# Performance work log

Hardware: AMD Instinct MI355X
Metric: run time of the kernel (lower is better)

Reference implementation:

```python
import jax, jax.numpy as jnp
import numpy as np

B, TI, TE, B_IN, B_OUT = 1024, 2, 3, 16, 32
DEGREES = (0, 2, 4, 6, 8)  # symmetric=True, l_in=8


def setup_inputs() -> dict:
    key = jax.random.key(0)
    ks = jax.random.split(key, 2 * len(DEGREES))
    inp = {}
    for i, l in enumerate(DEGREES):
        nsh = 2 * l + 1
        inp[f"x{l}"] = jax.random.normal(ks[2 * i], (B, TI, TE, B_IN, nsh), dtype=jnp.float32)
        inp[f"w{l}"] = jax.random.uniform(ks[2 * i + 1], (TI, TE, B_IN, B_OUT, nsh), dtype=jnp.float32) * 0.1
    inp["bias"] = jnp.zeros((1, TI, TE, B_OUT, 1, 1), dtype=jnp.float32)
    return inp


def reference(x0, x2, x4, x6, x8, w0, w2, w4, w6, w8, bias):
    xs = {0: x0, 2: x2, 4: x4, 6: x6, 8: x8}
    ws = {0: w0, 2: w2, 4: w4, 6: w6, 8: w8}
    rh = []
    for l in DEGREES:
        # (n,a,b,i,l) x (a,b,i,o,k) -> (n,a,b,o,l,k)
        out = jnp.einsum('nabil,abiok->nabolk', xs[l], ws[l])
        if l == 0:
            out = out + bias
        rh.append(out)
    return tuple(rh)
```

## Files before the change

### kernel.cpp

```cpp
#include <hip/hip_runtime.h>

#define B_    1024
#define AB_   6
#define BIN_  16
#define BOUT_ 32

typedef float f4 __attribute__((ext_vector_type(4)));
typedef _Float16 hlf4 __attribute__((ext_vector_type(4)));

template<int NSH, int SPB>
__device__ __forceinline__ void mfma_lds_body(const float* __restrict__ X,
                                              const float* __restrict__ W,
                                              float* __restrict__ OUT,
                                              float* os, int bi) {
    constexpr int SZ   = BIN_ * NSH;
    constexpr int NOUT = BOUT_ * NSH * NSH;
    constexpr int NT   = (BOUT_ * NSH) / 16;
    constexpr int MT   = (NSH + 15) / 16;
    constexpr int NTQ  = (NT + 3) / 4;

    const int tid  = threadIdx.x;
    const int lane = tid & 63;
    const int w    = tid >> 6;
    const int lm   = lane & 15;
    const int lk   = (lane >> 4) * 4;

    const int ab = bi % AB_;
    const int g  = bi / AB_;

    const float* Wab = W + (size_t)ab * (BIN_ * BOUT_ * NSH);

    hlf4 bfrag[NTQ];
#pragma unroll
    for (int t = 0; t < NTQ; ++t) {
        const int ni = w * NTQ + t;
        if (ni < NT) {
            const int n = ni * 16 + lm;
#pragma unroll
            for (int j = 0; j < 4; ++j)
                bfrag[t][j] = (_Float16)Wab[(lk + j) * (BOUT_ * NSH) + n];
        }
    }

    for (int s = 0; s < SPB; ++s) {
        const int slice = ab + AB_ * (g * SPB + s);
        const float* Xs = X + (size_t)slice * SZ;

        hlf4 afrag[MT];
#pragma unroll
        for (int mi = 0; mi < MT; ++mi) {
            const int l  = mi * 16 + lm;
            const int lc = (l > NSH - 1) ? (NSH - 1) : l;
#pragma unroll
            for (int j = 0; j < 4; ++j)
                afrag[mi][j] = (_Float16)Xs[(lk + j) * NSH + lc];
        }

#pragma unroll
        for (int t = 0; t < NTQ; ++t) {
            const int ni = w * NTQ + t;
            if (ni < NT) {
                const int n  = ni * 16 + lm;
                const int o  = n / NSH;
                const int kq = n - o * NSH;
                float* base = os + o * (NSH * NSH) + kq;
#pragma unroll
                for (int mi = 0; mi < MT; ++mi) {
                    f4 d = __builtin_amdgcn_mfma_f32_16x16x16f16(
                        afrag[mi], bfrag[t], (f4){0.f, 0.f, 0.f, 0.f}, 0, 0, 0);
#pragma unroll
                    for (int j = 0; j < 4; ++j) {
                        const int l = mi * 16 + lk + j;
                        if (l < NSH) base[l * NSH] = d[j];
                    }
                }
            }
        }
        __syncthreads();

        f4* dst = (f4*)(OUT + (size_t)slice * NOUT);
        const f4* src = (const f4*)os;
        for (int c = tid; c < NOUT / 4; c += 256) dst[c] = src[c];
        __syncthreads();
    }
}

__device__ __forceinline__ void l0_body(const float* __restrict__ X,
                                        const float* __restrict__ W,
                                        const float* __restrict__ bias,
                                        float* __restrict__ OUT, int b) {
    const int o  = threadIdx.x & 31;
    const int ns = threadIdx.x >> 5;
    const int n0 = (b / AB_) * 64;
    const int ab = b % AB_;
    float wv[BIN_];
#pragma unroll
    for (int i = 0; i < BIN_; ++i) wv[i] = W[(ab * BIN_ + i) * BOUT_ + o];
    const float bv = bias[ab * BOUT_ + o];
#pragma unroll
    for (int s = 0; s < 8; ++s) {
        const int n = n0 + ns + s * 8;
        const float* Xp = X + ((size_t)n * AB_ + ab) * BIN_;
        float acc = bv;
#pragma unroll
        for (int i = 0; i < BIN_; ++i) acc = fmaf(Xp[i], wv[i], acc);
        OUT[((size_t)n * AB_ + ab) * BOUT_ + o] = acc;
    }
}

#define NB8 768
#define NB6 768
#define NB4 768
#define NB2 768
#define NB0 96

__global__ __launch_bounds__(256, 4)
void s2conv_one(const float* __restrict__ x0, const float* __restrict__ x2,
                const float* __restrict__ x4, const float* __restrict__ x6,
                const float* __restrict__ x8,
                const float* __restrict__ w0, const float* __restrict__ w2,
                const float* __restrict__ w4, const float* __restrict__ w6,
                const float* __restrict__ w8,
                const float* __restrict__ bias, float* __restrict__ out,
                size_t off0, size_t off2, size_t off4, size_t off6, size_t off8) {
    __shared__ __attribute__((aligned(16))) float os[BOUT_ * 17 * 17];
    int b = blockIdx.x;
    if (b < NB8) { mfma_lds_body<17, 8>(x8, w8, out + off8, os, b); return; }
    b -= NB8;
    if (b < NB6) { mfma_lds_body<13, 8>(x6, w6, out + off6, os, b); return; }
    b -= NB6;
    if (b < NB4) { mfma_lds_body< 9, 8>(x4, w4, out + off4, os, b); return; }
    b -= NB4;
    if (b < NB2) { mfma_lds_body< 5, 8>(x2, w2, out + off2, os, b); return; }
    b -= NB2;
    l0_body(x0, w0, bias, out + off0, b);
}

extern "C" void kernel_launch(void* const* d_in, const int* in_sizes, int n_in,
                              void* d_out, int out_size, void* d_ws, size_t ws_size,
                              hipStream_t stream) {
    const float* x0 = (const float*)d_in[0];
    const float* w0 = (const float*)d_in[1];
    const float* x2 = (const float*)d_in[2];
    const float* w2 = (const float*)d_in[3];
    const float* x4 = (const float*)d_in[4];
    const float* w4 = (const float*)d_in[5];
    const float* x6 = (const float*)d_in[6];
    const float* w6 = (const float*)d_in[7];
    const float* x8 = (const float*)d_in[8];
    const float* w8 = (const float*)d_in[9];
    const float* bias = (const float*)d_in[10];
    float* out = (float*)d_out;

    const size_t per = (size_t)B_ * AB_ * BOUT_;
    size_t off0 = 0;
    size_t off2 = off0 + per * 1;
    size_t off4 = off2 + per * 25;
    size_t off6 = off4 + per * 81;
    size_t off8 = off6 + per * 169;

    const int nblocks = NB8 + NB6 + NB4 + NB2 + NB0;
    s2conv_one<<<nblocks, 256, 0, stream>>>(x0, x2, x4, x6, x8,
                                            w0, w2, w4, w6, w8,
                                            bias, out,
                                            off0, off2, off4, off6, off8);
}
```

Baseline: 112.5 us.

## Double-buffer LDS output staging and split large degrees into halves

Replaces the single LDS output staging buffer with two ping-pong buffers. The global store of one unit can then overlap the MFMA compute of the next, which removes one of the two barriers per slice. For degrees 6 and 8 the output channels are split into two halves per unit so that two half-size buffers fit in the same LDS budget. The next slice's input fragments are prefetched into registers. The cost is more registers for the extra weight fragments and the prefetched A, which may lower occupancy.

```diff
diff --git a/kernel.cpp b/kernel.cpp
--- a/kernel.cpp
+++ b/kernel.cpp
@@ -8,16 +8,19 @@
 typedef float f4 __attribute__((ext_vector_type(4)));
 typedef _Float16 hlf4 __attribute__((ext_vector_type(4)));
 
-template<int NSH, int SPB>
-__device__ __forceinline__ void mfma_lds_body(const float* __restrict__ X,
-                                              const float* __restrict__ W,
-                                              float* __restrict__ OUT,
-                                              float* os, int bi) {
-    constexpr int SZ   = BIN_ * NSH;
-    constexpr int NOUT = BOUT_ * NSH * NSH;
-    constexpr int NT   = (BOUT_ * NSH) / 16;
-    constexpr int MT   = (NSH + 15) / 16;
-    constexpr int NTQ  = (NT + 3) / 4;
+template<int NSH, int NHALF, int SPB>
+__device__ __forceinline__ void pipe_body(const float* __restrict__ X,
+                                          const float* __restrict__ W,
+                                          float* __restrict__ OUT,
+                                          float* os0, float* os1, int bi) {
+    constexpr int SZ    = BIN_ * NSH;
+    constexpr int NOUT  = BOUT_ * NSH * NSH;
+    constexpr int OPB   = BOUT_ / NHALF;
+    constexpr int USZ   = OPB * NSH * NSH;
+    constexpr int NTU   = (OPB * NSH) / 16;
+    constexpr int NTQ   = (NTU + 3) / 4;
+    constexpr int MT    = (NSH + 15) / 16;
+    constexpr int UNITS = SPB * NHALF;
 
     const int tid  = threadIdx.x;
     const int lane = tid & 63;
@@ -27,47 +30,51 @@
 
     const int ab = bi % AB_;
     const int g  = bi / AB_;
+    const int s0 = g * SPB;
 
     const float* Wab = W + (size_t)ab * (BIN_ * BOUT_ * NSH);
 
-    hlf4 bfrag[NTQ];
-#pragma unroll
-    for (int t = 0; t < NTQ; ++t) {
-        const int ni = w * NTQ + t;
-        if (ni < NT) {
-            const int n = ni * 16 + lm;
-#pragma unroll
-            for (int j = 0; j < 4; ++j)
-                bfrag[t][j] = (_Float16)Wab[(lk + j) * (BOUT_ * NSH) + n];
-        }
-    }
-
-    for (int s = 0; s < SPB; ++s) {
-        const int slice = ab + AB_ * (g * SPB + s);
-        const float* Xs = X + (size_t)slice * SZ;
-
-        hlf4 afrag[MT];
+    hlf4 bfrag[NHALF][NTQ];
+#pragma unroll
+    for (int h = 0; h < NHALF; ++h)
+#pragma unroll
+        for (int t = 0; t < NTQ; ++t) {
+            const int ni = w * NTQ + t;
+            if (ni < NTU) {
+                const int n = h * (OPB * NSH) + ni * 16 + lm;
+#pragma unroll
+                for (int j = 0; j < 4; ++j)
+                    bfrag[h][t][j] = (_Float16)Wab[(lk + j) * (BOUT_ * NSH) + n];
+            }
+        }
+
+    hlf4 acur[MT], anext[MT];
+
+    auto load_a = [&](int t, hlf4* dst) {
+        const float* Xs = X + (size_t)(ab + AB_ * t) * SZ;
 #pragma unroll
         for (int mi = 0; mi < MT; ++mi) {
             const int l  = mi * 16 + lm;
             const int lc = (l > NSH - 1) ? (NSH - 1) : l;
 #pragma unroll
             for (int j = 0; j < 4; ++j)
-                afrag[mi][j] = (_Float16)Xs[(lk + j) * NSH + lc];
-        }
-
+                dst[mi][j] = (_Float16)Xs[(lk + j) * NSH + lc];
+        }
+    };
+
+    auto compute = [&](int hh, float* buf) {
 #pragma unroll
         for (int t = 0; t < NTQ; ++t) {
             const int ni = w * NTQ + t;
-            if (ni < NT) {
-                const int n  = ni * 16 + lm;
-                const int o  = n / NSH;
-                const int kq = n - o * NSH;
-                float* base = os + o * (NSH * NSH) + kq;
+            if (ni < NTU) {
+                const int nl = ni * 16 + lm;
+                const int ol = nl / NSH;
+                const int kq = nl - ol * NSH;
+                float* base = buf + ol * (NSH * NSH) + kq;
 #pragma unroll
                 for (int mi = 0; mi < MT; ++mi) {
                     f4 d = __builtin_amdgcn_mfma_f32_16x16x16f16(
-                        afrag[mi], bfrag[t], (f4){0.f, 0.f, 0.f, 0.f}, 0, 0, 0);
+                        acur[mi], bfrag[hh][t], (f4){0.f, 0.f, 0.f, 0.f}, 0, 0, 0);
 #pragma unroll
                     for (int j = 0; j < 4; ++j) {
                         const int l = mi * 16 + lk + j;
@@ -76,13 +83,39 @@
                 }
             }
         }
+    };
+
+    auto flush = [&](int t, int hh, const float* buf) {
+        f4* dst = (f4*)(OUT + (size_t)(ab + AB_ * t) * NOUT + (size_t)hh * USZ);
+        const f4* src = (const f4*)buf;
+        for (int c = tid; c < USZ / 4; c += 256) dst[c] = src[c];
+    };
+
+    load_a(s0, acur);
+    if (SPB > 1) load_a(s0 + 1, anext);
+    compute(0, os0);
+
+    for (int u = 1; u < UNITS; ++u) {
         __syncthreads();
-
-        f4* dst = (f4*)(OUT + (size_t)slice * NOUT);
-        const f4* src = (const f4*)os;
-        for (int c = tid; c < NOUT / 4; c += 256) dst[c] = src[c];
-        __syncthreads();
+        const int s  = u / NHALF;
+        const int h  = u % NHALF;
+        const int ps = (u - 1) / NHALF;
+        const int ph = (u - 1) % NHALF;
+
+        if (h == 0) {
+#pragma unroll
+            for (int mi = 0; mi < MT; ++mi) acur[mi] = anext[mi];
+        }
+
+        flush(s0 + ps, ph, (u & 1) ? os0 : os1);
+
+        if (h == 0 && s + 1 < SPB) load_a(s0 + s + 1, anext);
+
+        if (NHALF == 2 && h == 1) compute(1, (u & 1) ? os1 : os0);
+        else                      compute(0, (u & 1) ? os1 : os0);
     }
+    __syncthreads();
+    flush(s0 + SPB - 1, NHALF - 1, ((UNITS - 1) & 1) ? os1 : os0);
 }
 
 __device__ __forceinline__ void l0_body(const float* __restrict__ X,
@@ -113,6 +146,7 @@
 #define NB4 768
 #define NB2 768
 #define NB0 96
+#define UMAX (16 * 17 * 17)
 
 __global__ __launch_bounds__(256, 4)
 void s2conv_one(const float* __restrict__ x0, const float* __restrict__ x2,
@@ -123,15 +157,15 @@
                 const float* __restrict__ w8,
                 const float* __restrict__ bias, float* __restrict__ out,
                 size_t off0, size_t off2, size_t off4, size_t off6, size_t off8) {
-    __shared__ __attribute__((aligned(16))) float os[BOUT_ * 17 * 17];
+    __shared__ __attribute__((aligned(16))) float os[2 * UMAX];
     int b = blockIdx.x;
-    if (b < NB8) { mfma_lds_body<17, 8>(x8, w8, out + off8, os, b); return; }
+    if (b < NB8) { pipe_body<17, 2, 8>(x8, w8, out + off8, os, os + UMAX, b); return; }
     b -= NB8;
-    if (b < NB6) { mfma_lds_body<13, 8>(x6, w6, out + off6, os, b); return; }
+    if (b < NB6) { pipe_body<13, 2, 8>(x6, w6, out + off6, os, os + UMAX, b); return; }
     b -= NB6;
-    if (b < NB4) { mfma_lds_body< 9, 8>(x4, w4, out + off4, os, b); return; }
+    if (b < NB4) { pipe_body< 9, 1, 8>(x4, w4, out + off4, os, os + UMAX, b); return; }
     b -= NB4;
-    if (b < NB2) { mfma_lds_body< 5, 8>(x2, w2, out + off2, os, b); return; }
+    if (b < NB2) { pipe_body< 5, 1, 8>(x2, w2, out + off2, os, os + UMAX, b); return; }
     b -= NB2;
     l0_body(x0, w0, bias, out + off0, b);
 }
```

Result: no change. 112.9 us (+0.4%).
